# Kernel optimization log

Hardware: AMD Instinct MI355X
Metric: run time of the kernel (lower is better)

The kernel has to match this reference:

```python
import jax, jax.numpy as jnp
import numpy as np

B, S, E, H = 4, 2048, 1024, 16
DH = E // H


def setup_inputs() -> dict:
    key = jax.random.key(0)
    ks = jax.random.split(key, 8)
    sc = 0.02
    inp = {
        "v": jax.random.normal(ks[0], (B, S, E), jnp.float32),
        "k": jax.random.normal(ks[1], (B, S, E), jnp.float32),
        "q": jax.random.normal(ks[2], (B, S, E), jnp.float32),
        # causal mask, broadcast over batch and heads; 0 => masked
        "mask": jnp.tril(jnp.ones((S, S), jnp.int32))[None, None, :, :],
        "wq": jax.random.normal(ks[3], (E, E), jnp.float32) * sc,
        "bq": jnp.zeros((E,), jnp.float32),
        "wk": jax.random.normal(ks[4], (E, E), jnp.float32) * sc,
        "bk": jnp.zeros((E,), jnp.float32),
        "wv": jax.random.normal(ks[5], (E, E), jnp.float32) * sc,
        "bv": jnp.zeros((E,), jnp.float32),
        "wo": jax.random.normal(ks[6], (E, E), jnp.float32) * sc,
        "bo": jnp.zeros((E,), jnp.float32),
    }
    return inp


def _split_heads(x):
    # [B,S,E] -> [B,H,S,DH]
    b, s, _ = x.shape
    return x.reshape(b, s, H, DH).transpose(0, 2, 1, 3)


def reference(v, k, q, mask, wq, bq, wk, bk, wv, bv, wo, bo):
    # Linear layers (torch Linear: x @ W^T + b)
    qh = _split_heads(q @ wq.T + bq)
    kh = _split_heads(k @ wk.T + bk)
    vh = _split_heads(v @ wv.T + bv)
    scale = 1.0 / jnp.sqrt(jnp.asarray(DH, qh.dtype))
    scores = jnp.einsum("bhqd,bhkd->bhqk", qh, kh) * scale  # [B,H,S,S]
    scores = jnp.where(mask == 0, -jnp.inf, scores)
    attn = jax.nn.softmax(scores, axis=-1)
    # dropout p=0.0 -> identity
    x = jnp.einsum("bhqk,bhkd->bhqd", attn, vh)  # [B,H,S,DH]
    x = x.transpose(0, 2, 1, 3).reshape(x.shape[0], -1, E)  # [B,S,E]
    return x @ wo.T + bo
```

## Files before the change

kernel.cpp:

```cpp
#include <hip/hip_runtime.h>
#include <hip/hip_bf16.h>

#define B_  4
#define S_  2048
#define E_  1024
#define H_  16
#define DH_ 64
constexpr int M_ = B_ * S_;
constexpr int K_ = E_;
constexpr int N_ = E_;
constexpr long NE_ = (long)B_ * S_ * E_;
constexpr long EE_ = (long)E_ * E_;

typedef __attribute__((ext_vector_type(8))) short bf16x8;
typedef __attribute__((ext_vector_type(4))) float f32x4;

__device__ __forceinline__ unsigned short f2bf(float f) {
    union { float f; unsigned u; } a; a.f = f;
    unsigned u = a.u;
    return (unsigned short)((u + 0x7fffu + ((u >> 16) & 1u)) >> 16);
}
__device__ __forceinline__ unsigned short f2bf_fast(float f) {
    union { float f; unsigned u; } a; a.f = f;
    return (unsigned short)((a.u + 0x8000u) >> 16);
}

__device__ __forceinline__ void async_copy16(const unsigned short* g, unsigned short* l) {
    __builtin_amdgcn_global_load_lds(
        (const __attribute__((address_space(1))) void*)g,
        (__attribute__((address_space(3))) void*)l, 16, 0, 0);
}

__global__ void cast3(const float* __restrict__ i0, const float* __restrict__ i1,
                      const float* __restrict__ i2,
                      unsigned short* __restrict__ o0, unsigned short* __restrict__ o1,
                      unsigned short* __restrict__ o2, int n4) {
    const float* in = blockIdx.y == 0 ? i0 : (blockIdx.y == 1 ? i1 : i2);
    unsigned short* out = blockIdx.y == 0 ? o0 : (blockIdx.y == 1 ? o1 : o2);
    int i = blockIdx.x * blockDim.x + threadIdx.x;
    if (i >= n4) return;
    float4 v = ((const float4*)in)[i];
    ushort4 o;
    o.x = f2bf(v.x); o.y = f2bf(v.y); o.z = f2bf(v.z); o.w = f2bf(v.w);
    ((ushort4*)out)[i] = o;
}

__global__ void cast4(const float* __restrict__ i0, const float* __restrict__ i1,
                      const float* __restrict__ i2, const float* __restrict__ i3,
                      unsigned short* __restrict__ o0, unsigned short* __restrict__ o1,
                      unsigned short* __restrict__ o2, unsigned short* __restrict__ o3,
                      int n4) {
    int y = blockIdx.y;
    const float* in = y == 0 ? i0 : (y == 1 ? i1 : (y == 2 ? i2 : i3));
    unsigned short* out = y == 0 ? o0 : (y == 1 ? o1 : (y == 2 ? o2 : o3));
    int i = blockIdx.x * blockDim.x + threadIdx.x;
    if (i >= n4) return;
    float4 v = ((const float4*)in)[i];
    ushort4 o;
    o.x = f2bf(v.x); o.y = f2bf(v.y); o.z = f2bf(v.z); o.w = f2bf(v.w);
    ((ushort4*)out)[i] = o;
}

__device__ __forceinline__ void gemm_core(
    const unsigned short* __restrict__ A, const unsigned short* __restrict__ Bw,
    unsigned short* sA, unsigned short* sB, int bm, int bn,
    int wave, int lane, f32x4 (*acc)[4]) {
    const int lane15 = lane & 15;
    const int laneq  = lane >> 4;
    const int waveM = wave & 1, waveN = wave >> 1;
    const int lrow = lane >> 3;
    const int lcol = (lane & 7) * 8;

    for (int k0 = 0; k0 < K_; k0 += 64) {
        __syncthreads();
        for (int c = wave; c < 16; c += 4) {
            const unsigned short* gA = A + (long)(bm * 128 + c * 8 + lrow) * K_ + k0 + lcol;
            async_copy16(gA, &sA[c * 512]);
            const unsigned short* gB = Bw + (long)(bn * 128 + c * 8 + lrow) * K_ + k0 + lcol;
            async_copy16(gB, &sB[c * 512]);
        }
        __syncthreads();
#pragma unroll
        for (int ks = 0; ks < 2; ++ks) {
            const int kc = ks * 32 + laneq * 8;
            bf16x8 af[4], bfr[4];
#pragma unroll
            for (int mi = 0; mi < 4; ++mi)
                af[mi] = *(const bf16x8*)&sA[(waveM * 64 + mi * 16 + lane15) * 64 + kc];
#pragma unroll
            for (int ni = 0; ni < 4; ++ni)
                bfr[ni] = *(const bf16x8*)&sB[(waveN * 64 + ni * 16 + lane15) * 64 + kc];
#pragma unroll
            for (int mi = 0; mi < 4; ++mi)
#pragma unroll
                for (int ni = 0; ni < 4; ++ni)
                    acc[mi][ni] = __builtin_amdgcn_mfma_f32_16x16x32_bf16(
                        af[mi], bfr[ni], acc[mi][ni], 0, 0, 0);
        }
    }
}

__global__ __launch_bounds__(256, 2)
void gemm3(const unsigned short* __restrict__ A0, const unsigned short* __restrict__ A1,
           const unsigned short* __restrict__ A2,
           const unsigned short* __restrict__ W0, const unsigned short* __restrict__ W1,
           const unsigned short* __restrict__ W2,
           const float* __restrict__ b0, const float* __restrict__ b1,
           const float* __restrict__ b2,
           unsigned short* __restrict__ o0, unsigned short* __restrict__ o1,
           unsigned short* __restrict__ o2, float osc0) {
    __shared__ __align__(16) unsigned short sA[128 * 64];
    __shared__ __align__(16) unsigned short sB[128 * 64];
    const int z = blockIdx.z;
    const unsigned short* A  = z == 0 ? A0 : (z == 1 ? A1 : A2);
    const unsigned short* Bw = z == 0 ? W0 : (z == 1 ? W1 : W2);
    const float* bias        = z == 0 ? b0 : (z == 1 ? b1 : b2);
    unsigned short* Out      = z == 0 ? o0 : (z == 1 ? o1 : o2);
    const float oscale = z == 0 ? osc0 : 1.0f;

    const int tid = threadIdx.x, wave = tid >> 6, lane = tid & 63;
    const int lane15 = lane & 15, laneq = lane >> 4;
    const int bm = blockIdx.x, bn = blockIdx.y;
    const int waveM = wave & 1, waveN = wave >> 1;

    f32x4 acc[4][4] = {};
    gemm_core(A, Bw, sA, sB, bm, bn, wave, lane, acc);

#pragma unroll
    for (int mi = 0; mi < 4; ++mi) {
        const int mbase = bm * 128 + waveM * 64 + mi * 16 + laneq * 4;
#pragma unroll
        for (int ni = 0; ni < 4; ++ni) {
            const int n = bn * 128 + waveN * 64 + ni * 16 + lane15;
            const float bv = bias[n];
#pragma unroll
            for (int r = 0; r < 4; ++r) {
                const int m = mbase + r;
                const float v = (acc[mi][ni][r] + bv) * oscale;
                const int b = m >> 11, s = m & (S_ - 1);
                const int h = n >> 6, d = n & (DH_ - 1);
                long idx;
                if (z == 2) idx = ((long)(b * H_ + h) * DH_ + d) * S_ + s;
                else        idx = ((long)(b * H_ + h) * S_ + s) * DH_ + d;
                Out[idx] = f2bf(v);
            }
        }
    }
}

__global__ __launch_bounds__(256, 2)
void gemm_out(const unsigned short* __restrict__ A, const unsigned short* __restrict__ Bw,
              const float* __restrict__ bias, float* __restrict__ Out) {
    __shared__ __align__(16) unsigned short sA[128 * 64];
    __shared__ __align__(16) unsigned short sB[128 * 64];
    const int tid = threadIdx.x, wave = tid >> 6, lane = tid & 63;
    const int lane15 = lane & 15, laneq = lane >> 4;
    const int bm = blockIdx.x, bn = blockIdx.y;
    const int waveM = wave & 1, waveN = wave >> 1;

    f32x4 acc[4][4] = {};
    gemm_core(A, Bw, sA, sB, bm, bn, wave, lane, acc);

#pragma unroll
    for (int mi = 0; mi < 4; ++mi) {
        const int mbase = bm * 128 + waveM * 64 + mi * 16 + laneq * 4;
#pragma unroll
        for (int ni = 0; ni < 4; ++ni) {
            const int n = bn * 128 + waveN * 64 + ni * 16 + lane15;
            const float bv = bias[n];
#pragma unroll
            for (int r = 0; r < 4; ++r)
                Out[(long)(mbase + r) * N_ + n] = acc[mi][ni][r] + bv;
        }
    }
}

constexpr int ALDK = 72;

template <bool DIAG>
__device__ __forceinline__ void attn_tile(
    const bf16x8* qf, const unsigned short* sK, const unsigned short* sV,
    unsigned short* sP, int wave, int lane15, int laneq,
    f32x4* o_acc, float* rs) {
    f32x4 sc[4] = {};
#pragma unroll
    for (int ks = 0; ks < 2; ++ks) {
#pragma unroll
        for (int ct = 0; ct < 4; ++ct) {
            bf16x8 kf = *(const bf16x8*)&sK[(ct * 16 + lane15) * ALDK + ks * 32 + laneq * 8];
            sc[ct] = __builtin_amdgcn_mfma_f32_16x16x32_bf16(qf[ks], kf, sc[ct], 0, 0, 0);
        }
    }
    const int prow = wave * 16 + laneq * 4;
#pragma unroll
    for (int ct = 0; ct < 4; ++ct) {
        const int colsw = ((ct ^ laneq) & 3) * 16 + lane15;
#pragma unroll
        for (int r = 0; r < 4; ++r) {
            float s = sc[ct][r];
            if (DIAG) {
                const int colg = ct * 16 + lane15;
                if (colg > prow + r) s = -1e30f;
            }
            const float p = __builtin_amdgcn_exp2f(s);
            rs[r] += p;
            sP[(prow + r) * ALDK + colsw] = f2bf_fast(p);
        }
    }
    const int pkey = ((lane15 >> 2) & 3) * 16;
#pragma unroll
    for (int ks = 0; ks < 2; ++ks) {
        const int pcol = (ks * 32 + laneq * 8) ^ pkey;
        bf16x8 pf = *(const bf16x8*)&sP[(wave * 16 + lane15) * ALDK + pcol];
#pragma unroll
        for (int dt = 0; dt < 4; ++dt) {
            bf16x8 vf = *(const bf16x8*)&sV[(dt * 16 + lane15) * ALDK + ks * 32 + laneq * 8];
            o_acc[dt] = __builtin_amdgcn_mfma_f32_16x16x32_bf16(pf, vf, o_acc[dt], 0, 0, 0);
        }
    }
}

__global__ __launch_bounds__(256, 4)
void attn_kernel(const unsigned short* __restrict__ qh,
                 const unsigned short* __restrict__ kh,
                 const unsigned short* __restrict__ vT,
                 unsigned short* __restrict__ ctx) {
    __shared__ __align__(16) unsigned short sK[2][64 * ALDK];
    __shared__ __align__(16) unsigned short sV[2][64 * ALDK];
    __shared__ __align__(16) unsigned short sP[64 * ALDK];

    const int tid = threadIdx.x;
    const int wave = tid >> 6, lane = tid & 63;
    const int lane15 = lane & 15, laneq = lane >> 4;
    const int x = blockIdx.x;
    const int qta = x, qtb = 31 - x;
    const int bh = blockIdx.y;
    const long headQ = (long)bh * S_ * DH_;
    const long headV = (long)bh * DH_ * S_;
    const int q0a = qta * 64, q0b = qtb * 64;

    bf16x8 qfA[2], qfB[2];
    {
        const unsigned short* qa = qh + headQ + (long)(q0a + wave * 16 + lane15) * DH_;
        qfA[0] = *(const bf16x8*)(qa + laneq * 8);
        qfA[1] = *(const bf16x8*)(qa + 32 + laneq * 8);
        const unsigned short* qbp = qh + headQ + (long)(q0b + wave * 16 + lane15) * DH_;
        qfB[0] = *(const bf16x8*)(qbp + laneq * 8);
        qfB[1] = *(const bf16x8*)(qbp + 32 + laneq * 8);
    }

    f32x4 oA[4] = {}, oB[4] = {};
    float rsA[4] = {0.f, 0.f, 0.f, 0.f}, rsB[4] = {0.f, 0.f, 0.f, 0.f};

    const int r0 = tid >> 3;
    const int c0 = (tid & 7) * 8;

    const int ktmax = qtb + 1;

    {
        const unsigned short* kbase = kh + headQ;
        *(bf16x8*)&sK[0][r0 * ALDK + c0] = *(const bf16x8*)(kbase + (long)r0 * DH_ + c0);
        *(bf16x8*)&sK[0][(32 + r0) * ALDK + c0] = *(const bf16x8*)(kbase + (long)(32 + r0) * DH_ + c0);
        const unsigned short* vbase = vT + headV;
        *(bf16x8*)&sV[0][r0 * ALDK + c0] = *(const bf16x8*)(vbase + (long)r0 * S_ + c0);
        *(bf16x8*)&sV[0][(32 + r0) * ALDK + c0] = *(const bf16x8*)(vbase + (long)(32 + r0) * S_ + c0);
    }

    for (int kt = 0; kt < ktmax; ++kt) {
        const int cur = kt & 1, nxt = cur ^ 1;
        __syncthreads();

        bf16x8 kr0, kr1, vr0, vr1;
        const bool pfn = (kt + 1 < ktmax);
        if (pfn) {
            const int k0n = (kt + 1) * 64;
            const unsigned short* kbase = kh + headQ + (long)k0n * DH_;
            kr0 = *(const bf16x8*)(kbase + (long)r0 * DH_ + c0);
            kr1 = *(const bf16x8*)(kbase + (long)(32 + r0) * DH_ + c0);
            const unsigned short* vbase = vT + headV + k0n;
            vr0 = *(const bf16x8*)(vbase + (long)r0 * S_ + c0);
            vr1 = *(const bf16x8*)(vbase + (long)(32 + r0) * S_ + c0);
        }

        if (kt == qtb)
            attn_tile<true >(qfB, sK[cur], sV[cur], sP, wave, lane15, laneq, oB, rsB);
        else
            attn_tile<false>(qfB, sK[cur], sV[cur], sP, wave, lane15, laneq, oB, rsB);

        if (kt <= qta) {
            if (kt == qta)
                attn_tile<true >(qfA, sK[cur], sV[cur], sP, wave, lane15, laneq, oA, rsA);
            else
                attn_tile<false>(qfA, sK[cur], sV[cur], sP, wave, lane15, laneq, oA, rsA);
        }

        if (pfn) {
            *(bf16x8*)&sK[nxt][r0 * ALDK + c0] = kr0;
            *(bf16x8*)&sK[nxt][(32 + r0) * ALDK + c0] = kr1;
            *(bf16x8*)&sV[nxt][r0 * ALDK + c0] = vr0;
            *(bf16x8*)&sV[nxt][(32 + r0) * ALDK + c0] = vr1;
        }
    }

    float lA[4], lB[4];
#pragma unroll
    for (int r = 0; r < 4; ++r) {
        float va = rsA[r];
        va += __shfl_xor(va, 1); va += __shfl_xor(va, 2);
        va += __shfl_xor(va, 4); va += __shfl_xor(va, 8);
        lA[r] = va;
        float vb = rsB[r];
        vb += __shfl_xor(vb, 1); vb += __shfl_xor(vb, 2);
        vb += __shfl_xor(vb, 4); vb += __shfl_xor(vb, 8);
        lB[r] = vb;
    }

    const int b = bh >> 4, h = bh & 15;
#pragma unroll
    for (int dt = 0; dt < 4; ++dt) {
        const int d = h * 64 + dt * 16 + lane15;
#pragma unroll
        for (int r = 0; r < 4; ++r) {
            const int rowo = wave * 16 + laneq * 4 + r;
            ctx[((long)b * S_ + q0a + rowo) * E_ + d] = f2bf(oA[dt][r] / lA[r]);
            ctx[((long)b * S_ + q0b + rowo) * E_ + d] = f2bf(oB[dt][r] / lB[r]);
        }
    }
}

extern "C" void kernel_launch(void* const* d_in, const int* in_sizes, int n_in,
                              void* d_out, int out_size, void* d_ws, size_t ws_size,
                              hipStream_t stream) {
    const float* v_in = (const float*)d_in[0];
    const float* k_in = (const float*)d_in[1];
    const float* q_in = (const float*)d_in[2];
    const float* wq = (const float*)d_in[4];
    const float* bq = (const float*)d_in[5];
    const float* wk = (const float*)d_in[6];
    const float* bk = (const float*)d_in[7];
    const float* wv = (const float*)d_in[8];
    const float* bv = (const float*)d_in[9];
    const float* wo = (const float*)d_in[10];
    const float* bo = (const float*)d_in[11];

    unsigned short* qb   = (unsigned short*)d_ws;
    unsigned short* kb   = qb + NE_;
    unsigned short* vb   = kb + NE_;
    unsigned short* wqb  = vb + NE_;
    unsigned short* wkb  = wqb + EE_;
    unsigned short* wvb  = wkb + EE_;
    unsigned short* wob  = wvb + EE_;
    unsigned short* qhb  = wob + EE_;
    unsigned short* khb  = qhb + NE_;
    unsigned short* vTb  = khb + NE_;
    unsigned short* ctxb = qb;

    const int n4a = (int)(NE_ / 4);
    const int n4w = (int)(EE_ / 4);
    cast3<<<dim3(n4a / 256, 3), 256, 0, stream>>>(q_in, k_in, v_in, qb, kb, vb, n4a);
    cast4<<<dim3(n4w / 256, 4), 256, 0, stream>>>(wq, wk, wv, wo, wqb, wkb, wvb, wob, n4w);

    const float QSCALE = 0.125f * 1.44269504089f;

    gemm3<<<dim3(M_ / 128, N_ / 128, 3), 256, 0, stream>>>(
        qb, kb, vb, wqb, wkb, wvb, bq, bk, bv, qhb, khb, vTb, QSCALE);

    attn_kernel<<<dim3(16, B_ * H_), 256, 0, stream>>>(qhb, khb, vTb, ctxb);

    gemm_out<<<dim3(M_ / 128, N_ / 128), 256, 0, stream>>>(ctxb, wob, bo, (float*)d_out);
}
```

Measured before the change: 362.6 us.

## Repack causal attention query-tile pairs into 12 equal-work groups per head

New measurement: 376.0 us. 3.7% more time.

```diff
diff --git a/kernel.cpp b/kernel.cpp
--- a/kernel.cpp
+++ b/kernel.cpp
@@ -176,6 +176,7 @@
 }
 
 constexpr int ALDK = 72;
+constexpr int TILE_E = 64 * ALDK;
 
 template <bool DIAG>
 __device__ __forceinline__ void attn_tile(
@@ -220,23 +221,12 @@
     }
 }
 
-__global__ __launch_bounds__(256, 4)
-void attn_kernel(const unsigned short* __restrict__ qh,
-                 const unsigned short* __restrict__ kh,
-                 const unsigned short* __restrict__ vT,
-                 unsigned short* __restrict__ ctx) {
-    __shared__ __align__(16) unsigned short sK[2][64 * ALDK];
-    __shared__ __align__(16) unsigned short sV[2][64 * ALDK];
-    __shared__ __align__(16) unsigned short sP[64 * ALDK];
-
-    const int tid = threadIdx.x;
-    const int wave = tid >> 6, lane = tid & 63;
-    const int lane15 = lane & 15, laneq = lane >> 4;
-    const int x = blockIdx.x;
-    const int qta = x, qtb = 31 - x;
-    const int bh = blockIdx.y;
-    const long headQ = (long)bh * S_ * DH_;
-    const long headV = (long)bh * DH_ * S_;
+__device__ __forceinline__ void attn_pair(
+    int qta, int qtb, int b, int h, long headQ, long headV,
+    const unsigned short* __restrict__ qh, const unsigned short* __restrict__ kh,
+    const unsigned short* __restrict__ vT, unsigned short* __restrict__ ctx,
+    unsigned short* sK, unsigned short* sV, unsigned short* sP,
+    int wave, int lane15, int laneq, int sr0, int sc0) {
     const int q0a = qta * 64, q0b = qtb * 64;
 
     bf16x8 qfA[2], qfB[2];
@@ -252,22 +242,23 @@
     f32x4 oA[4] = {}, oB[4] = {};
     float rsA[4] = {0.f, 0.f, 0.f, 0.f}, rsB[4] = {0.f, 0.f, 0.f, 0.f};
 
-    const int r0 = tid >> 3;
-    const int c0 = (tid & 7) * 8;
-
     const int ktmax = qtb + 1;
+
+    __syncthreads();
 
     {
         const unsigned short* kbase = kh + headQ;
-        *(bf16x8*)&sK[0][r0 * ALDK + c0] = *(const bf16x8*)(kbase + (long)r0 * DH_ + c0);
-        *(bf16x8*)&sK[0][(32 + r0) * ALDK + c0] = *(const bf16x8*)(kbase + (long)(32 + r0) * DH_ + c0);
+        *(bf16x8*)&sK[sr0 * ALDK + sc0] = *(const bf16x8*)(kbase + (long)sr0 * DH_ + sc0);
+        *(bf16x8*)&sK[(32 + sr0) * ALDK + sc0] = *(const bf16x8*)(kbase + (long)(32 + sr0) * DH_ + sc0);
         const unsigned short* vbase = vT + headV;
-        *(bf16x8*)&sV[0][r0 * ALDK + c0] = *(const bf16x8*)(vbase + (long)r0 * S_ + c0);
-        *(bf16x8*)&sV[0][(32 + r0) * ALDK + c0] = *(const bf16x8*)(vbase + (long)(32 + r0) * S_ + c0);
+        *(bf16x8*)&sV[sr0 * ALDK + sc0] = *(const bf16x8*)(vbase + (long)sr0 * S_ + sc0);
+        *(bf16x8*)&sV[(32 + sr0) * ALDK + sc0] = *(const bf16x8*)(vbase + (long)(32 + sr0) * S_ + sc0);
     }
 
     for (int kt = 0; kt < ktmax; ++kt) {
         const int cur = kt & 1, nxt = cur ^ 1;
+        unsigned short* sKc = sK + cur * TILE_E;
+        unsigned short* sVc = sV + cur * TILE_E;
         __syncthreads();
 
         bf16x8 kr0, kr1, vr0, vr1;
@@ -275,30 +266,32 @@
         if (pfn) {
             const int k0n = (kt + 1) * 64;
             const unsigned short* kbase = kh + headQ + (long)k0n * DH_;
-            kr0 = *(const bf16x8*)(kbase + (long)r0 * DH_ + c0);
-            kr1 = *(const bf16x8*)(kbase + (long)(32 + r0) * DH_ + c0);
+            kr0 = *(const bf16x8*)(kbase + (long)sr0 * DH_ + sc0);
+            kr1 = *(const bf16x8*)(kbase + (long)(32 + sr0) * DH_ + sc0);
             const unsigned short* vbase = vT + headV + k0n;
-            vr0 = *(const bf16x8*)(vbase + (long)r0 * S_ + c0);
-            vr1 = *(const bf16x8*)(vbase + (long)(32 + r0) * S_ + c0);
+            vr0 = *(const bf16x8*)(vbase + (long)sr0 * S_ + sc0);
+            vr1 = *(const bf16x8*)(vbase + (long)(32 + sr0) * S_ + sc0);
         }
 
         if (kt == qtb)
-            attn_tile<true >(qfB, sK[cur], sV[cur], sP, wave, lane15, laneq, oB, rsB);
+            attn_tile<true >(qfB, sKc, sVc, sP, wave, lane15, laneq, oB, rsB);
         else
-            attn_tile<false>(qfB, sK[cur], sV[cur], sP, wave, lane15, laneq, oB, rsB);
+            attn_tile<false>(qfB, sKc, sVc, sP, wave, lane15, laneq, oB, rsB);
 
         if (kt <= qta) {
             if (kt == qta)
-                attn_tile<true >(qfA, sK[cur], sV[cur], sP, wave, lane15, laneq, oA, rsA);
+                attn_tile<true >(qfA, sKc, sVc, sP, wave, lane15, laneq, oA, rsA);
             else
-                attn_tile<false>(qfA, sK[cur], sV[cur], sP, wave, lane15, laneq, oA, rsA);
+                attn_tile<false>(qfA, sKc, sVc, sP, wave, lane15, laneq, oA, rsA);
         }
 
         if (pfn) {
-            *(bf16x8*)&sK[nxt][r0 * ALDK + c0] = kr0;
-            *(bf16x8*)&sK[nxt][(32 + r0) * ALDK + c0] = kr1;
-            *(bf16x8*)&sV[nxt][r0 * ALDK + c0] = vr0;
-            *(bf16x8*)&sV[nxt][(32 + r0) * ALDK + c0] = vr1;
+            unsigned short* sKn = sK + nxt * TILE_E;
+            unsigned short* sVn = sV + nxt * TILE_E;
+            *(bf16x8*)&sKn[sr0 * ALDK + sc0] = kr0;
+            *(bf16x8*)&sKn[(32 + sr0) * ALDK + sc0] = kr1;
+            *(bf16x8*)&sVn[sr0 * ALDK + sc0] = vr0;
+            *(bf16x8*)&sVn[(32 + sr0) * ALDK + sc0] = vr1;
         }
     }
 
@@ -315,7 +308,6 @@
         lB[r] = vb;
     }
 
-    const int b = bh >> 4, h = bh & 15;
 #pragma unroll
     for (int dt = 0; dt < 4; ++dt) {
         const int d = h * 64 + dt * 16 + lane15;
@@ -325,6 +317,38 @@
             ctx[((long)b * S_ + q0a + rowo) * E_ + d] = f2bf(oA[dt][r] / lA[r]);
             ctx[((long)b * S_ + q0b + rowo) * E_ + d] = f2bf(oB[dt][r] / lB[r]);
         }
+    }
+}
+
+__global__ __launch_bounds__(256, 4)
+void attn_kernel(const unsigned short* __restrict__ qh,
+                 const unsigned short* __restrict__ kh,
+                 const unsigned short* __restrict__ vT,
+                 unsigned short* __restrict__ ctx) {
+    __shared__ __align__(16) unsigned short sK[2][64 * ALDK];
+    __shared__ __align__(16) unsigned short sV[2][64 * ALDK];
+    __shared__ __align__(16) unsigned short sP[64 * ALDK];
+
+    const int tid = threadIdx.x;
+    const int wave = tid >> 6, lane = tid & 63;
+    const int lane15 = lane & 15, laneq = lane >> 4;
+    const int g = blockIdx.x;
+    const int bh = blockIdx.y;
+    const long headQ = (long)bh * S_ * DH_;
+    const long headV = (long)bh * DH_ * S_;
+    const int b = bh >> 4, h = bh & 15;
+
+    const int sr0 = tid >> 3;
+    const int sc0 = (tid & 7) * 8;
+
+    const int cnt = g < 10 ? 1 : (g == 10 ? 2 : 4);
+    for (int i = 0; i < cnt; ++i) {
+        int qa, qb;
+        if (g < 10)       { qa = 11 + g;          qb = 31 - g; }
+        else if (g == 10) { qa = i == 0 ? 10 : 0; qb = i == 0 ? 21 : 9; }
+        else              { qa = 7 - 2 * i;       qb = 8 - 2 * i; }
+        attn_pair(qa, qb, b, h, headQ, headV, qh, kh, vT, ctx,
+                  &sK[0][0], &sV[0][0], sP, wave, lane15, laneq, sr0, sc0);
     }
 }
 
@@ -365,7 +389,7 @@
     gemm3<<<dim3(M_ / 128, N_ / 128, 3), 256, 0, stream>>>(
         qb, kb, vb, wqb, wkb, wvb, bq, bk, bv, qhb, khb, vTb, QSCALE);
 
-    attn_kernel<<<dim3(16, B_ * H_), 256, 0, stream>>>(qhb, khb, vTb, ctxb);
+    attn_kernel<<<dim3(12, B_ * H_), 256, 0, stream>>>(qhb, khb, vTb, ctxb);
 
     gemm_out<<<dim3(M_ / 128, N_ / 128), 256, 0, stream>>>(ctxb, wob, bo, (float*)d_out);
 }
```
